# Kernel tuning notes

Measured on AMD Instinct MI355X. Metric: run time of the kernel, lower is better.

Reference implementation:

```python
import jax, jax.numpy as jnp
import numpy as np

BASE_MARGIN = 0.1
N = 8192


def setup_inputs() -> dict:
    key = jax.random.key(0)
    k1, k2, k3 = jax.random.split(key, 3)
    predictions = jax.random.normal(k1, (N,), dtype=jnp.float32)
    targets = jax.random.normal(k2, (N,), dtype=jnp.float32)
    uncertainties = jax.random.uniform(k3, (N,), dtype=jnp.float32)
    return {"predictions": predictions, "targets": targets, "uncertainties": uncertainties}


def reference(predictions, targets, uncertainties):
    n = predictions.shape[0]
    # pairwise differences, [n, n]; entry (i, j) corresponds to pair (i, j)
    tdiff = targets[:, None] - targets[None, :]
    pdiff = predictions[:, None] - predictions[None, :]
    # adaptive margin: base_margin * clamp(|t_i - t_j|, 0.1, 1.0)
    margin = BASE_MARGIN * jnp.clip(jnp.abs(tdiff), 0.1, 1.0)
    # uncertainty weight: 1 / (1 + u_i + u_j)
    weight = 1.0 / (1.0 + uncertainties[:, None] + uncertainties[None, :])
    # if t_i > t_j: hinge(p_j - p_i + margin) = hinge(-pdiff + margin)
    # if t_j > t_i: hinge(p_i - p_j + margin) = hinge(+pdiff + margin)
    sgn = jnp.sign(tdiff)
    hinge = jnp.maximum(-sgn * pdiff + margin, 0.0)
    # only upper-triangular pairs (i < j) with t_i != t_j contribute
    iu = jnp.triu(jnp.ones((n, n), dtype=bool), k=1)
    mask = iu & (tdiff != 0.0)
    loss = jnp.sum(jnp.where(mask, weight * hinge, 0.0))
    count = jnp.sum(mask)
    return loss / jnp.maximum(count, 1).astype(loss.dtype)
```

## Files before the change

### kernel.cpp

```cpp
#include <hip/hip_runtime.h>


constexpr int TILE = 128;

template<bool DIAG>
__device__ __forceinline__ void tile_loop(
    const float* __restrict__ pred, const float* __restrict__ targ,
    const float* __restrict__ unc, int i, int j0,
    float pi, float ti, float ui1, float& acc, float& cntf)
{
    #pragma unroll 8
    for (int jj = 0; jj < TILE; ++jj) {
        const int jg = j0 + jj;
        const float tj = targ[jg];
        const float pj = pred[jg];
        const float uj = unc[jg];
        const float tdiff = ti - tj;
        const float pdiff = pi - pj;
        const float m3 = __builtin_amdgcn_fmed3f(fabsf(tdiff), 0.1f, 1.0f);
        const float spd = __uint_as_float(__float_as_uint(pdiff) ^
                                          (__float_as_uint(tdiff) & 0x80000000u));
        const float h = fmaxf(fmaf(m3, 0.1f, -spd), 0.0f);
        const float w = __builtin_amdgcn_rcpf(ui1 + uj);
        bool use = (tdiff != 0.0f);
        if (DIAG) use = use && (jg > i);
        acc  = fmaf(use ? w : 0.0f, h, acc);
        cntf += use ? 1.0f : 0.0f;
    }
}

__global__ __launch_bounds__(TILE) void arl_pair_kernel(
    const float* __restrict__ pred, const float* __restrict__ targ,
    const float* __restrict__ unc, int n, float2* __restrict__ partials)
{
    const int it = blockIdx.x;
    const int jt = blockIdx.y;
    const int bLin = jt * gridDim.x + it;

    float acc = 0.0f, cntf = 0.0f;

    if (jt >= it) {
        const int i  = it * TILE + threadIdx.x;
        const int j0 = jt * TILE;
        if (i < n) {
            const float pi  = pred[i];
            const float ti  = targ[i];
            const float ui1 = 1.0f + unc[i];
            if (j0 + TILE <= n) {
                if (it == jt) tile_loop<true >(pred, targ, unc, i, j0, pi, ti, ui1, acc, cntf);
                else          tile_loop<false>(pred, targ, unc, i, j0, pi, ti, ui1, acc, cntf);
            } else {
                const int jmax = n - j0;
                for (int jj = 0; jj < jmax; ++jj) {
                    const int jg = j0 + jj;
                    const float tdiff = ti - targ[jg];
                    const float pdiff = pi - pred[jg];
                    const float m3 = __builtin_amdgcn_fmed3f(fabsf(tdiff), 0.1f, 1.0f);
                    const float spd = __uint_as_float(__float_as_uint(pdiff) ^
                                                      (__float_as_uint(tdiff) & 0x80000000u));
                    const float h = fmaxf(fmaf(m3, 0.1f, -spd), 0.0f);
                    const float w = __builtin_amdgcn_rcpf(ui1 + unc[jg]);
                    const bool use = (tdiff != 0.0f) && (jg > i);
                    acc  = fmaf(use ? w : 0.0f, h, acc);
                    cntf += use ? 1.0f : 0.0f;
                }
            }
        }
        for (int off = 32; off > 0; off >>= 1) {
            acc  += __shfl_down(acc, off);
            cntf += __shfl_down(cntf, off);
        }
        __shared__ float sa[TILE / 64], sc[TILE / 64];
        const int lane = threadIdx.x & 63, wid = threadIdx.x >> 6;
        if (lane == 0) { sa[wid] = acc; sc[wid] = cntf; }
        __syncthreads();
        if (threadIdx.x == 0) {
            float a2 = 0.0f, c2 = 0.0f;
            #pragma unroll
            for (int w = 0; w < TILE / 64; ++w) { a2 += sa[w]; c2 += sc[w]; }
            partials[bLin] = float2{a2, c2};
        }
    } else {
        if (threadIdx.x == 0) partials[bLin] = float2{0.0f, 0.0f};
    }
}

__global__ __launch_bounds__(256) void arl_finalize(
    const float2* __restrict__ partials, int nPartials, float* __restrict__ out)
{
    float a = 0.0f, c = 0.0f;
    for (int k = threadIdx.x; k < nPartials; k += 256) {
        const float2 v = partials[k];
        a += v.x; c += v.y;
    }
    for (int off = 32; off > 0; off >>= 1) {
        a += __shfl_down(a, off);
        c += __shfl_down(c, off);
    }
    __shared__ float sa[4], sc[4];
    const int lane = threadIdx.x & 63, wid = threadIdx.x >> 6;
    if (lane == 0) { sa[wid] = a; sc[wid] = c; }
    __syncthreads();
    if (threadIdx.x == 0) {
        double A = 0.0, C = 0.0;
        #pragma unroll
        for (int w = 0; w < 4; ++w) { A += (double)sa[w]; C += (double)sc[w]; }
        out[0] = (float)(A / (C > 0.0 ? C : 1.0));
    }
}

extern "C" void kernel_launch(void* const* d_in, const int* in_sizes, int n_in,
                              void* d_out, int out_size, void* d_ws, size_t ws_size,
                              hipStream_t stream) {
    const float* pred = (const float*)d_in[0];
    const float* targ = (const float*)d_in[1];
    const float* unc  = (const float*)d_in[2];
    const int n = in_sizes[0];

    const int nt = (n + TILE - 1) / TILE;
    float2* partials = (float2*)d_ws;

    dim3 grid(nt, nt);
    arl_pair_kernel<<<grid, TILE, 0, stream>>>(pred, targ, unc, n, partials);
    arl_finalize<<<1, 256, 0, stream>>>(partials, nt * nt, (float*)d_out);
}
```

Baseline: 84.97 us.

## Launch only upper-triangular tiles and stage j-tile data in shared memory

```diff
diff --git a/kernel.cpp b/kernel.cpp
--- a/kernel.cpp
+++ b/kernel.cpp
@@ -3,85 +3,86 @@
 
 constexpr int TILE = 128;
 
-template<bool DIAG>
-__device__ __forceinline__ void tile_loop(
-    const float* __restrict__ pred, const float* __restrict__ targ,
-    const float* __restrict__ unc, int i, int j0,
-    float pi, float ti, float ui1, float& acc, float& cntf)
+__device__ __forceinline__ void pair_op(float pi, float ti, float ui1,
+                                        const float4& v, bool extra_ok,
+                                        float& acc, float& cntf)
 {
-    #pragma unroll 8
-    for (int jj = 0; jj < TILE; ++jj) {
-        const int jg = j0 + jj;
-        const float tj = targ[jg];
-        const float pj = pred[jg];
-        const float uj = unc[jg];
-        const float tdiff = ti - tj;
-        const float pdiff = pi - pj;
-        const float m3 = __builtin_amdgcn_fmed3f(fabsf(tdiff), 0.1f, 1.0f);
-        const float spd = __uint_as_float(__float_as_uint(pdiff) ^
-                                          (__float_as_uint(tdiff) & 0x80000000u));
-        const float h = fmaxf(fmaf(m3, 0.1f, -spd), 0.0f);
-        const float w = __builtin_amdgcn_rcpf(ui1 + uj);
-        bool use = (tdiff != 0.0f);
-        if (DIAG) use = use && (jg > i);
-        acc  = fmaf(use ? w : 0.0f, h, acc);
-        cntf += use ? 1.0f : 0.0f;
-    }
+    const float tdiff = ti - v.x;
+    const float pdiff = pi - v.y;
+    const float m3 = __builtin_amdgcn_fmed3f(fabsf(tdiff), 0.1f, 1.0f);
+    const float spd = __uint_as_float(__float_as_uint(pdiff) ^
+                                      (__float_as_uint(tdiff) & 0x80000000u));
+    const float h = fmaxf(fmaf(m3, 0.1f, -spd), 0.0f);
+    const float w = __builtin_amdgcn_rcpf(ui1 + v.z);
+    const bool use = (tdiff != 0.0f) && extra_ok;
+    acc  = fmaf(use ? w : 0.0f, h, acc);
+    cntf += use ? 1.0f : 0.0f;
 }
 
 __global__ __launch_bounds__(TILE) void arl_pair_kernel(
     const float* __restrict__ pred, const float* __restrict__ targ,
-    const float* __restrict__ unc, int n, float2* __restrict__ partials)
+    const float* __restrict__ unc, int n, int nt,
+    float2* __restrict__ partials)
 {
-    const int it = blockIdx.x;
-    const int jt = blockIdx.y;
-    const int bLin = jt * gridDim.x + it;
+    const int k = blockIdx.x;
+    int r = (int)((float)nt + 0.5f - sqrtf(((float)nt + 0.5f) * ((float)nt + 0.5f)
+                                           - 2.0f * (float)k));
+    if (r < 0) r = 0;
+    auto base = [nt](int rr) { return rr * nt - (rr * (rr - 1)) / 2; };
+    while (base(r + 1) <= k) ++r;
+    while (base(r) > k) --r;
+    const int c = r + (k - base(r));
+
+    const int tid = threadIdx.x;
+    const int i   = r * TILE + tid;
+    const int j0  = c * TILE;
+
+    __shared__ float4 sj[TILE];
+    {
+        const int jg = j0 + tid;
+        const bool v = jg < n;
+        sj[tid] = make_float4(v ? targ[jg] : 0.0f, v ? pred[jg] : 0.0f,
+                              v ? unc[jg] : 0.0f, 0.0f);
+    }
+    __syncthreads();
 
     float acc = 0.0f, cntf = 0.0f;
+    const bool full = (j0 + TILE <= n) && (r * TILE + TILE <= n);
 
-    if (jt >= it) {
-        const int i  = it * TILE + threadIdx.x;
-        const int j0 = jt * TILE;
-        if (i < n) {
-            const float pi  = pred[i];
-            const float ti  = targ[i];
-            const float ui1 = 1.0f + unc[i];
-            if (j0 + TILE <= n) {
-                if (it == jt) tile_loop<true >(pred, targ, unc, i, j0, pi, ti, ui1, acc, cntf);
-                else          tile_loop<false>(pred, targ, unc, i, j0, pi, ti, ui1, acc, cntf);
+    if (i < n) {
+        const float pi  = pred[i];
+        const float ti  = targ[i];
+        const float ui1 = 1.0f + unc[i];
+        if (full) {
+            if (r != c) {
+                #pragma unroll 8
+                for (int jj = 0; jj < TILE; ++jj)
+                    pair_op(pi, ti, ui1, sj[jj], true, acc, cntf);
             } else {
-                const int jmax = n - j0;
-                for (int jj = 0; jj < jmax; ++jj) {
-                    const int jg = j0 + jj;
-                    const float tdiff = ti - targ[jg];
-                    const float pdiff = pi - pred[jg];
-                    const float m3 = __builtin_amdgcn_fmed3f(fabsf(tdiff), 0.1f, 1.0f);
-                    const float spd = __uint_as_float(__float_as_uint(pdiff) ^
-                                                      (__float_as_uint(tdiff) & 0x80000000u));
-                    const float h = fmaxf(fmaf(m3, 0.1f, -spd), 0.0f);
-                    const float w = __builtin_amdgcn_rcpf(ui1 + unc[jg]);
-                    const bool use = (tdiff != 0.0f) && (jg > i);
-                    acc  = fmaf(use ? w : 0.0f, h, acc);
-                    cntf += use ? 1.0f : 0.0f;
-                }
+                #pragma unroll 8
+                for (int jj = 0; jj < TILE; ++jj)
+                    pair_op(pi, ti, ui1, sj[jj], (j0 + jj) > i, acc, cntf);
             }
+        } else {
+            const int jmax = (n - j0 < TILE) ? (n - j0) : TILE;
+            for (int jj = 0; jj < jmax; ++jj)
+                pair_op(pi, ti, ui1, sj[jj], (j0 + jj) > i, acc, cntf);
         }
-        for (int off = 32; off > 0; off >>= 1) {
-            acc  += __shfl_down(acc, off);
-            cntf += __shfl_down(cntf, off);
-        }
-        __shared__ float sa[TILE / 64], sc[TILE / 64];
-        const int lane = threadIdx.x & 63, wid = threadIdx.x >> 6;
-        if (lane == 0) { sa[wid] = acc; sc[wid] = cntf; }
-        __syncthreads();
-        if (threadIdx.x == 0) {
-            float a2 = 0.0f, c2 = 0.0f;
-            #pragma unroll
-            for (int w = 0; w < TILE / 64; ++w) { a2 += sa[w]; c2 += sc[w]; }
-            partials[bLin] = float2{a2, c2};
-        }
-    } else {
-        if (threadIdx.x == 0) partials[bLin] = float2{0.0f, 0.0f};
+    }
+
+    for (int off = 32; off > 0; off >>= 1) {
+        acc  += __shfl_down(acc, off);
+        cntf += __shfl_down(cntf, off);
+    }
+    __shared__ float sa[TILE / 64], sc[TILE / 64];
+    const int lane = tid & 63, wid = tid >> 6;
+    if (lane == 0) { sa[wid] = acc; sc[wid] = cntf; }
+    __syncthreads();
+    if (tid == 0) {
+        float a2 = 0.0f, c2 = 0.0f;
+        #pragma unroll
+        for (int w = 0; w < TILE / 64; ++w) { a2 += sa[w]; c2 += sc[w]; }
+        partials[k] = float2{a2, c2};
     }
 }
 
@@ -118,9 +119,9 @@
     const int n = in_sizes[0];
 
     const int nt = (n + TILE - 1) / TILE;
+    const int nTiles = nt * (nt + 1) / 2;
     float2* partials = (float2*)d_ws;
 
-    dim3 grid(nt, nt);
-    arl_pair_kernel<<<grid, TILE, 0, stream>>>(pred, targ, unc, n, partials);
-    arl_finalize<<<1, 256, 0, stream>>>(partials, nt * nt, (float*)d_out);
+    arl_pair_kernel<<<nTiles, TILE, 0, stream>>>(pred, targ, unc, n, nt, partials);
+    arl_finalize<<<1, 256, 0, stream>>>(partials, nTiles, (float*)d_out);
 }
```

Result: faster. 75.81 us (-10.8%).
